# Optimization experiments

Hardware: AMD Instinct MI355X
Metric: run time of the kernel (lower is better)

Reference implementation:

```python
import jax, jax.numpy as jnp
import numpy as np

B, S, H1, H2, D4, LAT, DD1, DD2, K = 8192, 4096, 196, 10, 1024, 32, 1024, 2048, 21

def _knn_mask(rng, rows, cols, k):
    # disjoint-group style mask: each column has exactly k ones (as produced by knnLayer's non-overlap grouping)
    m = np.zeros((rows, cols), dtype=np.float32)
    order = np.argsort(rng.random((rows, cols)), axis=0)[:k]  # [k, cols]
    m[order, np.arange(cols)[None, :]] = 1.0
    return m

def _glorot(rng, shape):
    lim = np.sqrt(6.0 / (shape[0] + shape[1]))
    return (rng.uniform(-lim, lim, size=shape)).astype(np.float32)

def setup_inputs() -> dict:
    rng = np.random.default_rng(0)
    key = jax.random.key(0)
    x = jax.random.uniform(key, (B, S), dtype=jnp.float32)
    inp = {
        'x': x,
        'C1': jnp.asarray(_knn_mask(rng, S, H1, K)),
        'W1': jnp.asarray(_glorot(rng, (S, H1))),
        'b1': jnp.zeros((H1,), jnp.float32),
        'C2': jnp.asarray(_knn_mask(rng, H1, H2, K)),
        'W2': jnp.asarray(_glorot(rng, (H1, H2))),
        'b2': jnp.zeros((H2,), jnp.float32),
        'W3': jnp.asarray(_glorot(rng, (H2, D4))),
        'b3': jnp.zeros((D4,), jnp.float32),
        'W4': jnp.asarray(_glorot(rng, (D4, LAT))),
        'b4': jnp.zeros((LAT,), jnp.float32),
        'Wd1': jnp.asarray(_glorot(rng, (LAT, DD1))),
        'bd1': jnp.zeros((DD1,), jnp.float32),
        'Wd2': jnp.asarray(_glorot(rng, (DD1, DD2))),
        'bd2': jnp.zeros((DD2,), jnp.float32),
        'Wd3': jnp.asarray(_glorot(rng, (DD2, S))),
        'bd3': jnp.zeros((S,), jnp.float32),
    }
    return inp

def reference(x, C1, W1, b1, C2, W2, b2, W3, b3, W4, b4, Wd1, bd1, Wd2, bd2, Wd3, bd3):
    # encoder: two masked (CustomConnected) layers + two dense layers
    h = jax.nn.relu(x @ (W1 * C1) + b1)            # [B, H1]
    h = jax.nn.relu(h @ (W2 * C2) + b2)            # [B, H2]
    h = jax.nn.relu(h @ W3 + b3)                    # [B, S/4]
    z = jax.nn.relu(h @ W4 + b4)                    # [B, latent]
    # decoder: relu, relu, sigmoid
    d = jax.nn.relu(z @ Wd1 + bd1)                  # [B, S/4]
    d = jax.nn.relu(d @ Wd2 + bd2)                  # [B, S/2]
    out = jax.nn.sigmoid(d @ Wd3 + bd3)             # [B, S]
    return out
```

## Files before the change

### kernel.cpp

```cpp
#include <hip/hip_runtime.h>
#include <hip/hip_fp8.h>
#include <cstdint>
#include <cstddef>

typedef __attribute__((ext_vector_type(4))) float f32x4;
typedef __attribute__((ext_vector_type(8))) int i32x8;

#define DEVINL __device__ __forceinline__

DEVINL unsigned short f2bf(float f){
  union { float f; unsigned u; } v; v.f = f;
  unsigned r = v.u + 0x7fffu + ((v.u >> 16) & 1u);
  return (unsigned short)(r >> 16);
}
DEVINL float bf2f(unsigned short h){
  union { unsigned u; float f; } v; v.u = ((unsigned)h) << 16;
  return v.f;
}
DEVINL unsigned char f2fp8(float f){
  __hip_fp8_e4m3 t(f);
  return (unsigned char)t.__x;
}
DEVINL void gload_lds16(const void* g, void* l){
  __builtin_amdgcn_global_load_lds((const __attribute__((address_space(1))) void*)g,
                                   (__attribute__((address_space(3))) void*)l, 16, 0, 0);
}

#define ACT_SCALE 64.0f
#define W_SCALE   16.0f
#define E8M0_ACT  121
#define E8M0_W    123

__global__ __launch_bounds__(256) void transpose_fp8(
    const float* __restrict__ W, unsigned char* __restrict__ Wt, int K, int N)
{
  __shared__ unsigned char tile[32][33];
  int k0 = blockIdx.x * 32, n0 = blockIdx.y * 32;
  int tx = threadIdx.x & 31, ty = threadIdx.x >> 5;
  #pragma unroll
  for (int i = 0; i < 4; ++i) {
    int k = k0 + ty + 8*i, n = n0 + tx;
    tile[ty + 8*i][tx] = f2fp8(W[(size_t)k*N + n] * W_SCALE);
  }
  __syncthreads();
  #pragma unroll
  for (int i = 0; i < 4; ++i) {
    int n = n0 + ty + 8*i, k = k0 + tx;
    Wt[(size_t)n*K + k] = tile[tx][ty + 8*i];
  }
}

__global__ __launch_bounds__(256) void build_sparse(
    const float* __restrict__ C1, const float* __restrict__ W1,
    unsigned* __restrict__ packed)
{
  const int j = blockIdx.x;
  const int w = threadIdx.x >> 6, l = threadIdx.x & 63;
  __shared__ int wcnt[4], wbase[4];
  int cnt = 0;
  #pragma unroll 4
  for (int it = 0; it < 16; ++it) {
    int k = w*1024 + it*64 + l;
    float c = C1[(size_t)k*196 + j];
    unsigned long long m = __ballot(c != 0.f);
    cnt += (int)__popcll(m);
  }
  if (l == 0) wcnt[w] = cnt;
  __syncthreads();
  if (threadIdx.x < 21) packed[j*21 + threadIdx.x] = 0;
  if (threadIdx.x == 0) {
    int b = 0;
    #pragma unroll
    for (int i = 0; i < 4; ++i) { wbase[i] = b; b += wcnt[i]; }
  }
  __syncthreads();
  int base = wbase[w];
  #pragma unroll 4
  for (int it = 0; it < 16; ++it) {
    int k = w*1024 + it*64 + l;
    float c = C1[(size_t)k*196 + j];
    unsigned long long m = __ballot(c != 0.f);
    if (c != 0.f) {
      int pos = base + (int)__popcll(m & ((1ull << l) - 1ull));
      if (pos < 21)
        packed[j*21 + pos] = ((unsigned)k << 16)
                           | (unsigned)f2bf(W1[(size_t)k*196 + j] * c);
    }
    base += (int)__popcll(m);
  }
}

__global__ __launch_bounds__(256) void layer1_sparse(
    const float* __restrict__ x, const unsigned* __restrict__ packed,
    const float* __restrict__ b1, unsigned short* __restrict__ h1)
{
  __shared__ __align__(16) float xs[2*4096];
  const int t = threadIdx.x;
  const long m0 = (long)blockIdx.x * 2;
  const char* src = (const char*)(x + m0*4096);
  #pragma unroll
  for (int i = 0; i < 8; ++i) {
    int seg = t + i*256;
    gload_lds16(src + (size_t)seg*16, (char*)xs + (size_t)seg*16);
  }
  __syncthreads();
  for (int e = t; e < 2*196; e += 256) {
    int row = (e >= 196) ? 1 : 0;
    int col = e - row*196;
    const float* xr = xs + row*4096;
    float acc = b1[col];
    #pragma unroll
    for (int i = 0; i < 21; ++i) {
      unsigned p = packed[col*21 + i];
      acc += xr[p >> 16] * bf2f((unsigned short)(p & 0xffffu));
    }
    h1[(m0 + row)*256 + col] = f2bf(fmaxf(acc, 0.f));
  }
}

template<int ACT>
__global__ __launch_bounds__(256, 2) void gemm_fp8(
    const unsigned char* __restrict__ A, const unsigned char* __restrict__ Bt,
    const float* __restrict__ bias, void* __restrict__ Cptr, int K, int ldC)
{
  constexpr int BM = 128, BN = 256, BK = 128;
  constexpr int FM = 8, FN = 4;
  __shared__ __align__(16) unsigned char smem[49152];
  unsigned char* As = smem;
  unsigned char* Bs = smem + 16384;
  const int tid  = threadIdx.x;
  const int lane = tid & 63;
  const int w    = tid >> 6;
  const int q = lane >> 4, l16 = lane & 15;
  const long m0 = (long)blockIdx.x * BM;
  const long n0 = (long)blockIdx.y * BN;

  f32x4 acc[FM][FN] = {};

  for (int k0 = 0; k0 < K; k0 += BK) {
    #pragma unroll
    for (int it = 0; it < 4; ++it) {
      int seg = tid + it*256;
      int row = seg >> 3;
      int g   = (5*(seg & 7) + 3*row) & 7;
      gload_lds16(A + (m0 + row)*(long)K + k0 + g*16, As + seg*16);
    }
    #pragma unroll
    for (int it = 0; it < 8; ++it) {
      int seg = tid + it*256;
      int row = seg >> 3;
      int g   = (5*(seg & 7) + 3*row) & 7;
      gload_lds16(Bt + (n0 + row)*(long)K + k0 + g*16, Bs + seg*16);
    }
    __syncthreads();

    i32x8 b[FN];
    #pragma unroll
    for (int j = 0; j < FN; ++j) {
      int r = w*64 + j*16 + l16;
      const uint4* p = (const uint4*)(Bs + r*BK);
      int c0 = (2*q + r) & 7;
      union { uint4 v[2]; i32x8 f; } u;
      u.v[0] = p[c0];
      u.v[1] = p[(c0 + 5) & 7];
      b[j] = u.f;
    }
    #pragma unroll
    for (int i = 0; i < FM; ++i) {
      int r = i*16 + l16;
      const uint4* p = (const uint4*)(As + r*BK);
      int c0 = (2*q + r) & 7;
      union { uint4 v[2]; i32x8 f; } u;
      u.v[0] = p[c0];
      u.v[1] = p[(c0 + 5) & 7];
      i32x8 a = u.f;
      #pragma unroll
      for (int j = 0; j < FN; ++j)
        acc[i][j] = __builtin_amdgcn_mfma_scale_f32_16x16x128_f8f6f4(
            a, b[j], acc[i][j], 0, 0, 0, E8M0_ACT, 0, E8M0_W);
    }
    __syncthreads();
  }

  if constexpr (ACT == 0) {
    #pragma unroll
    for (int j = 0; j < FN; ++j) {
      int cl = w*64 + j*16 + l16;
      float bv = bias[n0 + cl];
      #pragma unroll
      for (int i = 0; i < FM; ++i) {
        #pragma unroll
        for (int r = 0; r < 4; ++r) {
          int rl = i*16 + q*4 + r;
          smem[rl*272 + cl] = f2fp8(fmaxf(acc[i][j][r] + bv, 0.f) * ACT_SCALE);
        }
      }
    }
    __syncthreads();
    unsigned char* C = (unsigned char*)Cptr;
    #pragma unroll
    for (int it = 0; it < 8; ++it) {
      int seg = tid + it*256;
      int row = seg >> 4, ch = seg & 15;
      *(uint4*)(C + (m0 + row)*(long)ldC + n0 + ch*16) =
          *(const uint4*)(smem + row*272 + ch*16);
    }
  } else {
    float* C = (float*)Cptr;
    #pragma unroll
    for (int j = 0; j < FN; ++j) {
      long col = n0 + w*64 + j*16 + l16;
      float bv = bias[col];
      #pragma unroll
      for (int i = 0; i < FM; ++i) {
        #pragma unroll
        for (int r = 0; r < 4; ++r) {
          long row = m0 + i*16 + q*4 + r;
          float v = acc[i][j][r] + bv;
          C[row*(long)ldC + col] = 1.f / (1.f + __expf(-v));
        }
      }
    }
  }
}

__global__ __launch_bounds__(256) void layer2345(
    const unsigned short* __restrict__ h1,
    const float* __restrict__ W2, const float* __restrict__ C2, const float* __restrict__ b2,
    const float* __restrict__ W3, const float* __restrict__ b3,
    const float* __restrict__ W4, const float* __restrict__ b4,
    const float* __restrict__ Wd1, const float* __restrict__ bd1,
    unsigned char* __restrict__ d1)
{
  __shared__ float h1s[4][200];
  __shared__ float h2s[4][10];
  __shared__ float h3s[4][1024];
  __shared__ float part[8][128];
  __shared__ float zs[4][32];
  const int t = threadIdx.x;
  const int w = t >> 6, l = t & 63;
  const long m0 = (long)blockIdx.x * 4;

  for (int e = t; e < 4*196; e += 256) {
    int row = e / 196, col = e - row*196;
    h1s[row][col] = bf2f(h1[(m0 + row)*256 + col]);
  }
  __syncthreads();

  {
    float acc[10];
    #pragma unroll
    for (int n = 0; n < 10; ++n) acc[n] = 0.f;
    #pragma unroll
    for (int it = 0; it < 4; ++it) {
      int k = l + it*64;
      if (k < 196) {
        float a = h1s[w][k];
        #pragma unroll
        for (int n = 0; n < 10; ++n) acc[n] += a * W2[k*10 + n] * C2[k*10 + n];
      }
    }
    #pragma unroll
    for (int off = 32; off > 0; off >>= 1) {
      #pragma unroll
      for (int n = 0; n < 10; ++n) acc[n] += __shfl_down(acc[n], off, 64);
    }
    if (l < 10) h2s[w][l] = fmaxf(acc[l] + b2[l], 0.f);
  }
  __syncthreads();

  #pragma unroll
  for (int jj = 0; jj < 4; ++jj) {
    int n = w*256 + jj*64 + l;
    float a0 = b3[n], a1 = a0, a2 = a0, a3 = a0;
    #pragma unroll
    for (int k = 0; k < 10; ++k) {
      float wv = W3[k*1024 + n];
      a0 += h2s[0][k]*wv; a1 += h2s[1][k]*wv;
      a2 += h2s[2][k]*wv; a3 += h2s[3][k]*wv;
    }
    h3s[0][n] = fmaxf(a0, 0.f); h3s[1][n] = fmaxf(a1, 0.f);
    h3s[2][n] = fmaxf(a2, 0.f); h3s[3][n] = fmaxf(a3, 0.f);
  }
  __syncthreads();

  {
    int n = t & 31, kg = t >> 5;
    float a0 = 0.f, a1 = 0.f, a2 = 0.f, a3 = 0.f;
    for (int k = kg*128; k < kg*128 + 128; ++k) {
      float wv = W4[k*32 + n];
      a0 += h3s[0][k]*wv; a1 += h3s[1][k]*wv;
      a2 += h3s[2][k]*wv; a3 += h3s[3][k]*wv;
    }
    part[kg][0*32 + n] = a0; part[kg][1*32 + n] = a1;
    part[kg][2*32 + n] = a2; part[kg][3*32 + n] = a3;
  }
  __syncthreads();
  if (t < 128) {
    float s = 0.f;
    #pragma unroll
    for (int kg = 0; kg < 8; ++kg) s += part[kg][t];
    zs[t >> 5][t & 31] = fmaxf(s + b4[t & 31], 0.f);
  }
  __syncthreads();

  #pragma unroll
  for (int jj = 0; jj < 4; ++jj) {
    int n = w*256 + jj*64 + l;
    float a0 = bd1[n], a1 = a0, a2 = a0, a3 = a0;
    #pragma unroll
    for (int k = 0; k < 32; ++k) {
      float wv = Wd1[k*1024 + n];
      a0 += zs[0][k]*wv; a1 += zs[1][k]*wv;
      a2 += zs[2][k]*wv; a3 += zs[3][k]*wv;
    }
    d1[(m0 + 0)*1024 + n] = f2fp8(fmaxf(a0, 0.f) * ACT_SCALE);
    d1[(m0 + 1)*1024 + n] = f2fp8(fmaxf(a1, 0.f) * ACT_SCALE);
    d1[(m0 + 2)*1024 + n] = f2fp8(fmaxf(a2, 0.f) * ACT_SCALE);
    d1[(m0 + 3)*1024 + n] = f2fp8(fmaxf(a3, 0.f) * ACT_SCALE);
  }
}

extern "C" void kernel_launch(void* const* d_in, const int* in_sizes, int n_in,
                              void* d_out, int out_size, void* d_ws, size_t ws_size,
                              hipStream_t stream)
{
  (void)in_sizes; (void)n_in; (void)out_size; (void)ws_size;
  const float* x   = (const float*)d_in[0];
  const float* C1  = (const float*)d_in[1];
  const float* W1  = (const float*)d_in[2];
  const float* b1  = (const float*)d_in[3];
  const float* C2  = (const float*)d_in[4];
  const float* W2  = (const float*)d_in[5];
  const float* b2  = (const float*)d_in[6];
  const float* W3  = (const float*)d_in[7];
  const float* b3  = (const float*)d_in[8];
  const float* W4  = (const float*)d_in[9];
  const float* b4  = (const float*)d_in[10];
  const float* Wd1 = (const float*)d_in[11];
  const float* bd1 = (const float*)d_in[12];
  const float* Wd2 = (const float*)d_in[13];
  const float* bd2 = (const float*)d_in[14];
  const float* Wd3 = (const float*)d_in[15];
  const float* bd3 = (const float*)d_in[16];
  float* out = (float*)d_out;

  char* ws = (char*)d_ws;
  size_t off = 0;
  auto alloc = [&](size_t bytes) -> void* {
    void* p = ws + off; off += (bytes + 255) & ~(size_t)255; return p;
  };
  unsigned char* Wt2 = (unsigned char*)alloc((size_t)2048*1024);
  unsigned char* Wt3 = (unsigned char*)alloc((size_t)4096*2048);
  unsigned*      pk  = (unsigned*)     alloc((size_t)196*21*4);
  unsigned short* h1 = (unsigned short*)alloc((size_t)8192*256*2);
  unsigned char*  d1 = (unsigned char*) alloc((size_t)8192*1024);
  unsigned char*  d2 = (unsigned char*) alloc((size_t)8192*2048);

  build_sparse<<<dim3(196), 256, 0, stream>>>(C1, W1, pk);
  transpose_fp8<<<dim3(1024/32, 2048/32), 256, 0, stream>>>(Wd2, Wt2, 1024, 2048);
  transpose_fp8<<<dim3(2048/32, 4096/32), 256, 0, stream>>>(Wd3, Wt3, 2048, 4096);

  layer1_sparse<<<dim3(8192/2), 256, 0, stream>>>(x, pk, b1, h1);
  layer2345<<<dim3(8192/4), 256, 0, stream>>>(h1, W2, C2, b2, W3, b3, W4, b4,
                                              Wd1, bd1, d1);
  gemm_fp8<0><<<dim3(8192/128, 2048/256), 256, 0, stream>>>(
      d1, Wt2, bd2, d2, 1024, 2048);
  gemm_fp8<1><<<dim3(8192/128, 4096/256), 256, 0, stream>>>(
      d2, Wt3, bd3, out, 2048, 4096);
}
```

Baseline: 458.7 us.

## Enlarge FP8 GEMM tile to 256x256 with 512 threads and double-buffered LDS

Both FP8 GEMM kernels now use a 256x256 block tile with 8 waves arranged 2x4. The kernel takes 128KB of dynamic LDS so it can double-buffer the A/B k-slices and prefetch the next slice while the MFMAs work on the current one. The goal is to hide global-to-LDS latency and to raise operand reuse per block. In exchange, the large LDS footprint limits occupancy to one block per CU. The __launch_bounds__(512,2) hint also squeezes the register budget against the 128-float accumulator array, which risks spilling.

```diff
diff --git a/kernel.cpp b/kernel.cpp
--- a/kernel.cpp
+++ b/kernel.cpp
@@ -119,45 +119,57 @@
 }
 
 template<int ACT>
-__global__ __launch_bounds__(256, 2) void gemm_fp8(
+__global__ __launch_bounds__(512, 2) void gemm_fp8(
     const unsigned char* __restrict__ A, const unsigned char* __restrict__ Bt,
     const float* __restrict__ bias, void* __restrict__ Cptr, int K, int ldC)
 {
-  constexpr int BM = 128, BN = 256, BK = 128;
+  constexpr int BM = 256, BN = 256, BK = 128;
   constexpr int FM = 8, FN = 4;
-  __shared__ __align__(16) unsigned char smem[49152];
-  unsigned char* As = smem;
-  unsigned char* Bs = smem + 16384;
+  extern __shared__ unsigned char sm[];
   const int tid  = threadIdx.x;
   const int lane = tid & 63;
   const int w    = tid >> 6;
+  const int wm = w >> 2, wn = w & 3;
   const int q = lane >> 4, l16 = lane & 15;
   const long m0 = (long)blockIdx.x * BM;
   const long n0 = (long)blockIdx.y * BN;
 
   f32x4 acc[FM][FN] = {};
-
-  for (int k0 = 0; k0 < K; k0 += BK) {
+  const int NT = K >> 7;
+
+  auto stage = [&](int buf, int kk) {
+    unsigned char* As = sm + buf*65536;
+    unsigned char* Bs = As + 32768;
     #pragma unroll
     for (int it = 0; it < 4; ++it) {
-      int seg = tid + it*256;
+      int seg = tid + it*512;
       int row = seg >> 3;
       int g   = (5*(seg & 7) + 3*row) & 7;
-      gload_lds16(A + (m0 + row)*(long)K + k0 + g*16, As + seg*16);
-    }
-    #pragma unroll
-    for (int it = 0; it < 8; ++it) {
-      int seg = tid + it*256;
+      gload_lds16(A + (m0 + row)*(long)K + kk + g*16, As + seg*16);
+    }
+    #pragma unroll
+    for (int it = 0; it < 4; ++it) {
+      int seg = tid + it*512;
       int row = seg >> 3;
       int g   = (5*(seg & 7) + 3*row) & 7;
-      gload_lds16(Bt + (n0 + row)*(long)K + k0 + g*16, Bs + seg*16);
-    }
-    __syncthreads();
+      gload_lds16(Bt + (n0 + row)*(long)K + kk + g*16, Bs + seg*16);
+    }
+  };
+
+  stage(0, 0);
+  __syncthreads();
+
+  for (int t = 0; t < NT; ++t) {
+    int cur = t & 1;
+    if (t + 1 < NT) stage(cur ^ 1, (t + 1) << 7);
+
+    const unsigned char* As = sm + cur*65536;
+    const unsigned char* Bs = As + 32768;
 
     i32x8 b[FN];
     #pragma unroll
     for (int j = 0; j < FN; ++j) {
-      int r = w*64 + j*16 + l16;
+      int r = wn*64 + j*16 + l16;
       const uint4* p = (const uint4*)(Bs + r*BK);
       int c0 = (2*q + r) & 7;
       union { uint4 v[2]; i32x8 f; } u;
@@ -167,7 +179,7 @@
     }
     #pragma unroll
     for (int i = 0; i < FM; ++i) {
-      int r = i*16 + l16;
+      int r = wm*128 + i*16 + l16;
       const uint4* p = (const uint4*)(As + r*BK);
       int c0 = (2*q + r) & 7;
       union { uint4 v[2]; i32x8 f; } u;
@@ -185,14 +197,14 @@
   if constexpr (ACT == 0) {
     #pragma unroll
     for (int j = 0; j < FN; ++j) {
-      int cl = w*64 + j*16 + l16;
+      int cl = wn*64 + j*16 + l16;
       float bv = bias[n0 + cl];
       #pragma unroll
       for (int i = 0; i < FM; ++i) {
         #pragma unroll
         for (int r = 0; r < 4; ++r) {
-          int rl = i*16 + q*4 + r;
-          smem[rl*272 + cl] = f2fp8(fmaxf(acc[i][j][r] + bv, 0.f) * ACT_SCALE);
+          int rl = wm*128 + i*16 + q*4 + r;
+          sm[rl*272 + cl] = f2fp8(fmaxf(acc[i][j][r] + bv, 0.f) * ACT_SCALE);
         }
       }
     }
@@ -200,22 +212,22 @@
     unsigned char* C = (unsigned char*)Cptr;
     #pragma unroll
     for (int it = 0; it < 8; ++it) {
-      int seg = tid + it*256;
+      int seg = tid + it*512;
       int row = seg >> 4, ch = seg & 15;
       *(uint4*)(C + (m0 + row)*(long)ldC + n0 + ch*16) =
-          *(const uint4*)(smem + row*272 + ch*16);
+          *(const uint4*)(sm + row*272 + ch*16);
     }
   } else {
     float* C = (float*)Cptr;
     #pragma unroll
     for (int j = 0; j < FN; ++j) {
-      long col = n0 + w*64 + j*16 + l16;
+      long col = n0 + wn*64 + j*16 + l16;
       float bv = bias[col];
       #pragma unroll
       for (int i = 0; i < FM; ++i) {
         #pragma unroll
         for (int r = 0; r < 4; ++r) {
-          long row = m0 + i*16 + q*4 + r;
+          long row = m0 + wm*128 + i*16 + q*4 + r;
           float v = acc[i][j][r] + bv;
           C[row*(long)ldC + col] = 1.f / (1.f + __expf(-v));
         }
@@ -357,6 +369,15 @@
   unsigned char*  d1 = (unsigned char*) alloc((size_t)8192*1024);
   unsigned char*  d2 = (unsigned char*) alloc((size_t)8192*2048);
 
+  static int attr_set = 0;
+  if (!attr_set) {
+    hipFuncSetAttribute((const void*)gemm_fp8<0>,
+                        hipFuncAttributeMaxDynamicSharedMemorySize, 131072);
+    hipFuncSetAttribute((const void*)gemm_fp8<1>,
+                        hipFuncAttributeMaxDynamicSharedMemorySize, 131072);
+    attr_set = 1;
+  }
+
   build_sparse<<<dim3(196), 256, 0, stream>>>(C1, W1, pk);
   transpose_fp8<<<dim3(1024/32, 2048/32), 256, 0, stream>>>(Wd2, Wt2, 1024, 2048);
   transpose_fp8<<<dim3(2048/32, 4096/32), 256, 0, stream>>>(Wd3, Wt3, 2048, 4096);
@@ -364,8 +385,8 @@
   layer1_sparse<<<dim3(8192/2), 256, 0, stream>>>(x, pk, b1, h1);
   layer2345<<<dim3(8192/4), 256, 0, stream>>>(h1, W2, C2, b2, W3, b3, W4, b4,
                                               Wd1, bd1, d1);
-  gemm_fp8<0><<<dim3(8192/128, 2048/256), 256, 0, stream>>>(
+  gemm_fp8<0><<<dim3(8192/256, 2048/256), 512, 131072, stream>>>(
       d1, Wt2, bd2, d2, 1024, 2048);
-  gemm_fp8<1><<<dim3(8192/128, 4096/256), 256, 0, stream>>>(
+  gemm_fp8<1><<<dim3(8192/256, 4096/256), 512, 131072, stream>>>(
       d2, Wt3, bd3, out, 2048, 4096);
 }
```

Result: slower. 471.2 us (+2.7%).
